# Optimization experiments

Measured on AMD Instinct MI355X. Metric: run time of the kernel, lower is better.

The kernel has to match this reference:

```python
import jax, jax.numpy as jnp
import numpy as np

B, T, D, H, V, K = 64, 128, 300, 256, 30000, 16
FILTERS = [3, 4, 5]
FN = [100, 100, 100]
CLS = 5


def setup_inputs() -> dict:
    key = jax.random.key(0)
    ks = jax.random.split(key, 32)
    n = lambda i, shape, s=0.05: (jax.random.normal(ks[i], shape, jnp.float32) * s)
    inp = jax.random.randint(ks[0], (B, T), 0, V)
    emb = n(1, (V + 2, D)).at[V + 1].set(0.0)  # padding_idx row = 0
    # GRU (1 layer, bidirectional), PyTorch gate order r,z,n
    Wx_f, Wh_f = n(2, (3 * H, D)), n(3, (3 * H, H))
    bx_f, bh_f = n(4, (3 * H,)), n(5, (3 * H,))
    Wx_b, Wh_b = n(6, (3 * H, D)), n(7, (3 * H, H))
    bx_b, bh_b = n(8, (3 * H,)), n(9, (3 * H,))
    fc1c_W, fc1c_b = n(10, (D, 2 * H)), n(11, (D,))
    concept_table = n(12, (V, K, D), 0.1)
    counts = jax.random.randint(ks[13], (V,), 1, K + 1)
    concept_mask = (jnp.arange(K)[None, :] < counts[:, None])  # bool [V,K]
    conv_W0, conv_b0 = n(14, (FN[0], FILTERS[0] * 2 * D)), n(15, (FN[0],))
    conv_W1, conv_b1 = n(16, (FN[1], FILTERS[1] * 2 * D)), n(17, (FN[1],))
    conv_W2, conv_b2 = n(18, (FN[2], FILTERS[2] * 2 * D)), n(19, (FN[2],))
    fc1_W, fc1_b = n(20, (100, sum(FN))), n(21, (100,))
    fc2_W, fc2_b = n(22, (CLS, 100)), n(23, (CLS,))
    return dict(inp=inp, emb=emb, Wx_f=Wx_f, Wh_f=Wh_f, bx_f=bx_f, bh_f=bh_f,
                Wx_b=Wx_b, Wh_b=Wh_b, bx_b=bx_b, bh_b=bh_b,
                fc1c_W=fc1c_W, fc1c_b=fc1c_b,
                concept_table=concept_table, concept_mask=concept_mask,
                conv_W0=conv_W0, conv_b0=conv_b0, conv_W1=conv_W1, conv_b1=conv_b1,
                conv_W2=conv_W2, conv_b2=conv_b2,
                fc1_W=fc1_W, fc1_b=fc1_b, fc2_W=fc2_W, fc2_b=fc2_b)


def _gru_dir(x, Wx, Wh, bx, bh):
    # x: [B,T,D] -> hidden states [B,T,H]; PyTorch GRU cell math.
    xg = jnp.einsum('btd,gd->btg', x, Wx) + bx  # precompute input gates [B,T,3H]

    def step(h, xg_t):
        gh = h @ Wh.T + bh
        xr, xz, xn = jnp.split(xg_t, 3, axis=-1)
        hr, hz, hn = jnp.split(gh, 3, axis=-1)
        r = jax.nn.sigmoid(xr + hr)
        z = jax.nn.sigmoid(xz + hz)
        nn_ = jnp.tanh(xn + r * hn)
        h2 = (1.0 - z) * nn_ + z * h
        return h2, h2

    h0 = jnp.zeros((x.shape[0], Wh.shape[1]), x.dtype)
    _, ys = jax.lax.scan(step, h0, jnp.swapaxes(xg, 0, 1))
    return jnp.swapaxes(ys, 0, 1)


def _forward(inp, emb, Wx_f, Wh_f, bx_f, bh_f, Wx_b, Wh_b, bx_b, bh_b,
             fc1c_W, fc1c_b, concept_table, concept_mask,
             conv_W0, conv_b0, conv_W1, conv_b1, conv_W2, conv_b2,
             fc1_W, fc1_b, fc2_W, fc2_b):
    x = emb[inp]                                   # [B,T,D]
    hf = _gru_dir(x, Wx_f, Wh_f, bx_f, bh_f)
    hb = jnp.flip(_gru_dir(jnp.flip(x, 1), Wx_b, Wh_b, bx_b, bh_b), 1)
    out = jnp.concatenate([hf, hb], axis=-1)       # [B,T,2H]
    ctx = jnp.einsum('bth,dh->btd', out, fc1c_W) + fc1c_b  # [B,T,D] context
    # batched gather-attend-reduce over per-word concept lists
    conc = concept_table[inp]                      # [B,T,K,D]
    mask = concept_mask[inp]                       # [B,T,K] bool
    scores = jnp.einsum('btkd,btd->btk', conc, ctx)
    scores = jnp.where(mask, scores, jnp.float32(-1e30))
    attn = jax.nn.softmax(scores, axis=-1)
    concept = jnp.einsum('btk,btkd->btd', attn, conc)
    concept = jax.lax.stop_gradient(concept)       # original detaches via .data.numpy()
    feat = jnp.concatenate([ctx, concept], axis=-1)  # [B,T,2D]
    pooled = []
    for fs, W, b in ((FILTERS[0], conv_W0, conv_b0),
                     (FILTERS[1], conv_W1, conv_b1),
                     (FILTERS[2], conv_W2, conv_b2)):
        L = T - fs + 1
        # Conv1d(kernel=2D*fs, stride=2D) over flattened feat == token-window matmul
        win = jnp.concatenate([feat[:, i:i + L, :] for i in range(fs)], axis=-1)  # [B,L,fs*2D]
        c = jax.nn.relu(jnp.einsum('blk,fk->blf', win, W) + b)
        pooled.append(jnp.max(c, axis=1))          # max-pool over positions -> [B,FN]
    h = jnp.concatenate(pooled, axis=1)            # [B,300]; dropout is identity in eval
    h = h @ fc1_W.T + fc1_b
    h = h @ fc2_W.T + fc2_b
    return jax.nn.softmax(h, axis=1)


def reference(inp, emb, Wx_f, Wh_f, bx_f, bh_f, Wx_b, Wh_b, bx_b, bh_b,
              fc1c_W, fc1c_b, concept_table, concept_mask,
              conv_W0, conv_b0, conv_W1, conv_b1, conv_W2, conv_b2,
              fc1_W, fc1_b, fc2_W, fc2_b):
    return _forward(inp, emb, Wx_f, Wh_f, bx_f, bh_f, Wx_b, Wh_b, bx_b, bh_b,
                    fc1c_W, fc1c_b, concept_table, concept_mask,
                    conv_W0, conv_b0, conv_W1, conv_b1, conv_W2, conv_b2,
                    fc1_W, fc1_b, fc2_W, fc2_b)
```

## Files before the change

kernel.cpp:

```cpp
#include <hip/hip_runtime.h>


typedef unsigned short u16;
typedef unsigned int u32;
typedef __attribute__((ext_vector_type(4))) u16 u16x4;
typedef __attribute__((ext_vector_type(8))) u16 u16x8;
typedef __attribute__((ext_vector_type(8))) __bf16 bf16x8;
typedef __attribute__((ext_vector_type(4))) float f32x4;

__device__ __forceinline__ float bf2f(u16 u) {
    union { u32 i; float f; } x; x.i = ((u32)u) << 16; return x.f;
}
__device__ __forceinline__ u16 f2bf(float f) {
    union { float f; u32 i; } x; x.f = f;
    u32 r = x.i + 0x7FFFu + ((x.i >> 16) & 1u);
    return (u16)(r >> 16);
}
__device__ __forceinline__ float sigm(float x) { return 1.f / (1.f + __expf(-x)); }
__device__ __forceinline__ float tanh_(float x) {
    float e = __expf(-2.f * fabsf(x));
    float t = (1.f - e) / (1.f + e);
    return x < 0.f ? -t : t;
}

__global__ __launch_bounds__(256) void detect_k(
    const u32* __restrict__ emb_raw, const u32* __restrict__ cmask_raw,
    int* __restrict__ flags)
{
    __shared__ int cnt0, cnt1;
    if (threadIdx.x == 0) { cnt0 = 0; cnt1 = 0; }
    __syncthreads();
    int c0 = 0;
    for (int i = threadIdx.x; i < 4096; i += 256) {
        float lo = bf2f((u16)(emb_raw[i] & 0xFFFFu));
        if (!(fabsf(lo) <= 4.0f)) c0++;
    }
    int c1 = 0;
    for (int i = threadIdx.x; i < 1024; i += 256) {
        if (cmask_raw[i] > 1u) c1++;
    }
    if (c0) atomicAdd(&cnt0, c0);
    if (c1) atomicAdd(&cnt1, c1);
    __syncthreads();
    if (threadIdx.x == 0) {
        flags[0] = (cnt0 > 64) ? 1 : 0;
        flags[1] = (cnt1 > 0) ? 1 : 0;
    }
}

struct CvtDesc { const void* src; u16* dst; int n; };
struct CvtArgs { CvtDesc d[20]; };

__global__ __launch_bounds__(256) void convert_many(CvtArgs a, const int* __restrict__ flags)
{
    CvtDesc de = a.d[blockIdx.y];
    const bool f32m = flags[0] != 0;
    int i4 = (blockIdx.x * 256 + threadIdx.x) * 4;
    if (i4 >= de.n) return;
    if (i4 + 4 <= de.n) {
        if (f32m) {
            const float* s = (const float*)de.src + i4;
            u16x4 o; o[0] = f2bf(s[0]); o[1] = f2bf(s[1]); o[2] = f2bf(s[2]); o[3] = f2bf(s[3]);
            *(u16x4*)(de.dst + i4) = o;
        } else {
            *(u16x4*)(de.dst + i4) = *(const u16x4*)((const u16*)de.src + i4);
        }
    } else {
        for (int e = 0; e < 4 && i4 + e < de.n; ++e)
            de.dst[i4 + e] = f32m ? f2bf(((const float*)de.src)[i4 + e])
                                  : ((const u16*)de.src)[i4 + e];
    }
}

__global__ __launch_bounds__(256) void build_mask(
    const void* __restrict__ cmask, int* __restrict__ mask16, const int* __restrict__ flags)
{
    int v = blockIdx.x * 256 + threadIdx.x;
    if (v >= 30000) return;
    int m = 0;
    if (flags[1]) {
        const unsigned char* p = (const unsigned char*)cmask + (size_t)v * 16;
#pragma unroll
        for (int k = 0; k < 16; ++k) if (p[k]) m |= (1 << k);
    } else {
        const int* p = (const int*)cmask + (size_t)v * 16;
#pragma unroll
        for (int k = 0; k < 16; ++k) if (p[k]) m |= (1 << k);
    }
    mask16[v] = m;
}

template<int ROWMODE, int EPI, int OUTBF>
__global__ __launch_bounds__(256) void gemm_bt(
    const u16* __restrict__ A, const u16* __restrict__ W,
    const u16* __restrict__ bias, const int* __restrict__ rowidx,
    float* __restrict__ Cf, u16* __restrict__ Cb,
    int M, int N, int K, int lda, int ldc, int Lrows, int strideT)
{
    __shared__ __align__(16) u16 sA[64 * 40];
    __shared__ __align__(16) u16 sW[64 * 40];

    const int tid = threadIdx.x;
    const int m0 = blockIdx.y * 64;
    const int n0 = blockIdx.x * 64;

    const int l  = tid & 63;
    const int w  = tid >> 6;
    const int wm = (w >> 1) << 5;
    const int wn = (w & 1) << 5;
    const int fr = l & 15;
    const int fk = (l >> 4) << 3;

    const int sr = tid >> 2;
    const int cb = (tid & 3) << 3;

    size_t abase;
    {
        int m = m0 + sr;
        if constexpr (ROWMODE == 1) {
            abase = (size_t)rowidx[m] * (size_t)lda;
        } else if constexpr (ROWMODE == 2) {
            int b = m / Lrows; int li = m - b * Lrows;
            abase = (size_t)(b * strideT + li) * (size_t)lda;
        } else {
            abase = (size_t)m * (size_t)lda;
        }
    }
    const int  wrow   = n0 + sr;
    const bool wvalid = wrow < N;
    const size_t wbase = (size_t)wrow * (size_t)K;

    f32x4 acc00 = {0,0,0,0}, acc01 = {0,0,0,0}, acc10 = {0,0,0,0}, acc11 = {0,0,0,0};

    for (int k0 = 0; k0 < K; k0 += 32) {
        __syncthreads();
        {
            u16x4 v0 = {0,0,0,0}, v1 = {0,0,0,0};
            int k = k0 + cb;
            if (k + 8 <= K) {
                const u16* p = A + abase + k;
                v0 = *(const u16x4*)p;
                v1 = *(const u16x4*)(p + 4);
            } else {
#pragma unroll
                for (int e = 0; e < 4; ++e) { int kk = k + e;     if (kk < K) v0[e] = A[abase + kk]; }
#pragma unroll
                for (int e = 0; e < 4; ++e) { int kk = k + 4 + e; if (kk < K) v1[e] = A[abase + kk]; }
            }
            *(u16x4*)(sA + sr * 40 + cb)     = v0;
            *(u16x4*)(sA + sr * 40 + cb + 4) = v1;
        }
        {
            u16x4 v0 = {0,0,0,0}, v1 = {0,0,0,0};
            int k = k0 + cb;
            if (wvalid) {
                if (k + 8 <= K) {
                    const u16* p = W + wbase + k;
                    v0 = *(const u16x4*)p;
                    v1 = *(const u16x4*)(p + 4);
                } else {
#pragma unroll
                    for (int e = 0; e < 4; ++e) { int kk = k + e;     if (kk < K) v0[e] = W[wbase + kk]; }
#pragma unroll
                    for (int e = 0; e < 4; ++e) { int kk = k + 4 + e; if (kk < K) v1[e] = W[wbase + kk]; }
                }
            }
            *(u16x4*)(sW + sr * 40 + cb)     = v0;
            *(u16x4*)(sW + sr * 40 + cb + 4) = v1;
        }
        __syncthreads();

        bf16x8 a0 = *(const bf16x8*)(sA + (wm + fr)      * 40 + fk);
        bf16x8 a1 = *(const bf16x8*)(sA + (wm + 16 + fr) * 40 + fk);
        bf16x8 b0 = *(const bf16x8*)(sW + (wn + fr)      * 40 + fk);
        bf16x8 b1 = *(const bf16x8*)(sW + (wn + 16 + fr) * 40 + fk);

        acc00 = __builtin_amdgcn_mfma_f32_16x16x32_bf16(a0, b0, acc00, 0, 0, 0);
        acc01 = __builtin_amdgcn_mfma_f32_16x16x32_bf16(a0, b1, acc01, 0, 0, 0);
        acc10 = __builtin_amdgcn_mfma_f32_16x16x32_bf16(a1, b0, acc10, 0, 0, 0);
        acc11 = __builtin_amdgcn_mfma_f32_16x16x32_bf16(a1, b1, acc11, 0, 0, 0);
    }

    const int rb = (l >> 4) << 2;
    const int cc = l & 15;
#define EPILOG(ACC, I, J)                                                     \
    {                                                                         \
        int col = n0 + wn + (J)*16 + cc;                                      \
        if (col < N) {                                                        \
            float bv = bf2f(bias[col]);                                       \
            _Pragma("unroll")                                                 \
            for (int r = 0; r < 4; ++r) {                                     \
                int row = m0 + wm + (I)*16 + rb + r;                          \
                if (row < M) {                                                \
                    float v = ACC[r] + bv;                                    \
                    if (EPI == 2) v = fmaxf(v, 0.f);                          \
                    if (OUTBF) Cb[(size_t)row * ldc + col] = f2bf(v);         \
                    else       Cf[(size_t)row * ldc + col] = v;               \
                }                                                             \
            }                                                                 \
        }                                                                     \
    }
    EPILOG(acc00, 0, 0); EPILOG(acc01, 0, 1); EPILOG(acc10, 1, 0); EPILOG(acc11, 1, 1);
#undef EPILOG
}

#define GB 8
__global__ __launch_bounds__(512, 2) void gru_scan_mfma(
    const u16* __restrict__ xgf, const u16* __restrict__ xgb,
    const u16* __restrict__ whf, const u16* __restrict__ whb,
    const u16* __restrict__ bhf, const u16* __restrict__ bhb,
    u16* __restrict__ outb)
{
    const int bg  = blockIdx.x;
    const int dir = blockIdx.y;
    const u16* xg = dir ? xgb : xgf;
    const u16* wh = dir ? whb : whf;
    const u16* bh = dir ? bhb : bhf;

    const int tid = threadIdx.x;
    const int w = tid >> 6;
    const int l = tid & 63;

    __shared__ __align__(16) u16 h_bf[16][264];
    __shared__ __align__(16) float h_f[GB][260];
    __shared__ __align__(16) float gh[GB][772];
    __shared__ float bh_s[768];

    for (int i = tid; i < 16 * 264; i += 512) ((u16*)h_bf)[i] = 0;
    for (int i = tid; i < GB * 260; i += 512) ((float*)h_f)[i] = 0.f;
    for (int i = tid; i < 768; i += 512) bh_s[i] = bf2f(bh[i]);

    bf16x8 bfr[6][8];
#pragma unroll
    for (int c = 0; c < 6; ++c) {
#pragma unroll
        for (int kt = 0; kt < 8; ++kt) {
            const int n = w * 96 + c * 16 + (l & 15);
            const int k = kt * 32 + (l >> 4) * 8;
            bfr[c][kt] = *(const bf16x8*)(wh + (size_t)n * 256 + k);
        }
    }

    const int qrow = (l >> 4) << 2;
    const int arow = l & 15;
    const int aofs = (l >> 4) << 3;
    const int j0 = l * 4;
    const int bglob = bg * GB + w;

    __syncthreads();

    for (int s = 0; s < 128; ++s) {
        const int t = dir ? (127 - s) : s;

        f32x4 acc[6];
#pragma unroll
        for (int c = 0; c < 6; ++c) acc[c] = (f32x4){0.f, 0.f, 0.f, 0.f};
#pragma unroll
        for (int kt = 0; kt < 8; ++kt) {
            bf16x8 a = *(const bf16x8*)(&h_bf[arow][kt * 32 + aofs]);
#pragma unroll
            for (int c = 0; c < 6; ++c)
                acc[c] = __builtin_amdgcn_mfma_f32_16x16x32_bf16(a, bfr[c][kt], acc[c], 0, 0, 0);
        }
        if (qrow < GB) {
#pragma unroll
            for (int c = 0; c < 6; ++c) {
                const int col = w * 96 + c * 16 + (l & 15);
#pragma unroll
                for (int r = 0; r < 4; ++r)
                    gh[qrow + r][col] = acc[c][r];
            }
        }
        __syncthreads();

        const size_t tokbase = (size_t)(bglob * 128 + t) * 768;
        u16x4 xr4 = *(const u16x4*)(xg + tokbase + j0);
        u16x4 xz4 = *(const u16x4*)(xg + tokbase + 256 + j0);
        u16x4 xn4 = *(const u16x4*)(xg + tokbase + 512 + j0);
        f32x4 gr = *(const f32x4*)(&gh[w][j0]);
        f32x4 gz = *(const f32x4*)(&gh[w][256 + j0]);
        f32x4 gn = *(const f32x4*)(&gh[w][512 + j0]);
        f32x4 br = *(const f32x4*)(&bh_s[j0]);
        f32x4 bz = *(const f32x4*)(&bh_s[256 + j0]);
        f32x4 bn = *(const f32x4*)(&bh_s[512 + j0]);
        f32x4 hp = *(const f32x4*)(&h_f[w][j0]);
        u16x4 ho;
        f32x4 hn;
#pragma unroll
        for (int e = 0; e < 4; ++e) {
            float r = sigm(bf2f(xr4[e]) + gr[e] + br[e]);
            float z = sigm(bf2f(xz4[e]) + gz[e] + bz[e]);
            float n = tanh_(bf2f(xn4[e]) + r * (gn[e] + bn[e]));
            float h2 = (1.f - z) * n + z * hp[e];
            hn[e] = h2;
            ho[e] = f2bf(h2);
        }
        *(u16x4*)(&h_bf[w][j0]) = ho;
        *(f32x4*)(&h_f[w][j0]) = hn;
        *(u16x4*)(outb + (size_t)(bglob * 128 + t) * 512 + dir * 256 + j0) = ho;
        __syncthreads();
    }
}
#undef GB

__global__ __launch_bounds__(256) void attn_kernel(
    const int* __restrict__ inp, const void* __restrict__ ctab,
    const int* __restrict__ mask16, const int* __restrict__ flags,
    u16* __restrict__ feat)
{
    const int tok = blockIdx.x;
    const int tid = threadIdx.x;
    const int v = inp[tok];
    const bool f32m = flags[0] != 0;

    __shared__ float ctx_s[300];
    __shared__ __align__(16) u16 conc_s[16 * 300];
    __shared__ float sc_s[16];
    __shared__ float at_s[16];

    for (int d = tid; d < 300; d += 256) ctx_s[d] = bf2f(feat[(size_t)tok * 600 + d]);
    if (f32m) {
        const float4* src = (const float4*)((const float*)ctab + (size_t)v * 4800);
        for (int i = tid; i < 1200; i += 256) {
            float4 x = src[i];
            u16x4 o; o[0] = f2bf(x.x); o[1] = f2bf(x.y); o[2] = f2bf(x.z); o[3] = f2bf(x.w);
            *(u16x4*)(conc_s + i * 4) = o;
        }
    } else {
        const u16x8* src = (const u16x8*)((const u16*)ctab + (size_t)v * 4800);
        u16x8* dst = (u16x8*)conc_s;
        for (int i = tid; i < 600; i += 256) dst[i] = src[i];
    }
    __syncthreads();

    const int g = tid >> 4, ln = tid & 15;
    float s = 0.f;
    for (int d = ln; d < 300; d += 16) s += bf2f(conc_s[g * 300 + d]) * ctx_s[d];
    s += __shfl_xor(s, 1); s += __shfl_xor(s, 2); s += __shfl_xor(s, 4); s += __shfl_xor(s, 8);
    if (ln == 0) sc_s[g] = ((mask16[v] >> g) & 1) ? s : -1e30f;
    __syncthreads();

    if (tid == 0) {
        float m = -1e30f;
#pragma unroll
        for (int i = 0; i < 16; ++i) m = fmaxf(m, sc_s[i]);
        float p[16]; float den = 0.f;
#pragma unroll
        for (int i = 0; i < 16; ++i) {
            float pe = (sc_s[i] <= -1e29f) ? 0.f : __expf(sc_s[i] - m);
            p[i] = pe; den += pe;
        }
        float inv = den > 0.f ? 1.f / den : 0.f;
#pragma unroll
        for (int i = 0; i < 16; ++i) at_s[i] = p[i] * inv;
    }
    __syncthreads();

    for (int d = tid; d < 300; d += 256) {
        float a = 0.f;
#pragma unroll
        for (int g2 = 0; g2 < 16; ++g2) a += at_s[g2] * bf2f(conc_s[g2 * 300 + d]);
        feat[(size_t)tok * 600 + 300 + d] = f2bf(a);
    }
}

__global__ __launch_bounds__(128) void maxpool_k(
    const float* __restrict__ c0, const float* __restrict__ c1,
    const float* __restrict__ c2, float* __restrict__ pool)
{
    const int b = blockIdx.x, which = blockIdx.y, f = threadIdx.x;
    if (f >= 100) return;
    const float* c = which == 0 ? c0 : (which == 1 ? c1 : c2);
    const int L = which == 0 ? 126 : (which == 1 ? 125 : 124);
    float m = -1e30f;
    for (int l = 0; l < L; ++l) m = fmaxf(m, c[(size_t)(b * L + l) * 100 + f]);
    pool[b * 300 + which * 100 + f] = m;
}

__global__ __launch_bounds__(128) void final_k(
    const float* __restrict__ pool,
    const u16* __restrict__ fc1W, const u16* __restrict__ fc1b,
    const u16* __restrict__ fc2W, const u16* __restrict__ fc2b,
    float* __restrict__ out)
{
    const int b = blockIdx.x, tid = threadIdx.x;
    __shared__ float ps[300], h1[100], lg[5];
    for (int d = tid; d < 300; d += 128) ps[d] = pool[b * 300 + d];
    __syncthreads();
    if (tid < 100) {
        float a = bf2f(fc1b[tid]);
        for (int k = 0; k < 300; ++k) a += bf2f(fc1W[tid * 300 + k]) * ps[k];
        h1[tid] = a;
    }
    __syncthreads();
    if (tid < 5) {
        float a = bf2f(fc2b[tid]);
        for (int k = 0; k < 100; ++k) a += bf2f(fc2W[tid * 100 + k]) * h1[k];
        lg[tid] = a;
    }
    __syncthreads();
    if (tid == 0) {
        float m = fmaxf(fmaxf(fmaxf(lg[0], lg[1]), fmaxf(lg[2], lg[3])), lg[4]);
        float e0 = __expf(lg[0] - m), e1 = __expf(lg[1] - m), e2 = __expf(lg[2] - m),
              e3 = __expf(lg[3] - m), e4 = __expf(lg[4] - m);
        float inv = 1.f / (e0 + e1 + e2 + e3 + e4);
        out[b * 5 + 0] = e0 * inv;
        out[b * 5 + 1] = e1 * inv;
        out[b * 5 + 2] = e2 * inv;
        out[b * 5 + 3] = e3 * inv;
        out[b * 5 + 4] = e4 * inv;
    }
}

extern "C" void kernel_launch(void* const* d_in, const int* in_sizes, int n_in,
                              void* d_out, int out_size, void* d_ws, size_t ws_size,
                              hipStream_t stream)
{
    (void)n_in; (void)out_size; (void)ws_size;

    const int*  inp     = (const int*)d_in[0];
    const void* embR    = d_in[1];
    const void* WxfR    = d_in[2];
    const void* WhfR    = d_in[3];
    const void* bxfR    = d_in[4];
    const void* bhfR    = d_in[5];
    const void* WxbR    = d_in[6];
    const void* WhbR    = d_in[7];
    const void* bxbR    = d_in[8];
    const void* bhbR    = d_in[9];
    const void* fc1cWR  = d_in[10];
    const void* fc1cbR  = d_in[11];
    const void* ctabR   = d_in[12];
    const void* cmaskR  = d_in[13];
    const void* cw0R    = d_in[14];
    const void* cb0R    = d_in[15];
    const void* cw1R    = d_in[16];
    const void* cb1R    = d_in[17];
    const void* cw2R    = d_in[18];
    const void* cb2R    = d_in[19];
    const void* fc1WR   = d_in[20];
    const void* fc1bR   = d_in[21];
    const void* fc2WR   = d_in[22];
    const void* fc2bR   = d_in[23];

    char* ws = (char*)d_ws;
    size_t off = 0;
    auto alloc = [&](size_t bytes) -> char* {
        char* r = ws + off;
        off = (off + bytes + 255) & ~(size_t)255;
        return r;
    };

    u16*   xgf    = (u16*)alloc(8192ull * 768 * 2);
    u16*   xgb    = (u16*)alloc(8192ull * 768 * 2);
    u16*   outb   = (u16*)alloc(8192ull * 512 * 2);
    u16*   feat   = (u16*)alloc(8192ull * 600 * 2);
    float* c0     = (float*)alloc(64ull * 126 * 100 * 4);
    float* c1     = (float*)alloc(64ull * 125 * 100 * 4);
    float* c2     = (float*)alloc(64ull * 124 * 100 * 4);
    float* pool   = (float*)alloc(64ull * 300 * 4);
    int*   flags  = (int*)alloc(256);
    int*   mask16 = (int*)alloc(30000ull * 4);
    u16*   embc   = (u16*)alloc(9000600ull * 2);
    u16*   wxfc   = (u16*)alloc(230400ull * 2);
    u16*   whfc   = (u16*)alloc(196608ull * 2);
    u16*   bxfc   = (u16*)alloc(768ull * 2);
    u16*   bhfc   = (u16*)alloc(768ull * 2);
    u16*   wxbc   = (u16*)alloc(230400ull * 2);
    u16*   whbc   = (u16*)alloc(196608ull * 2);
    u16*   bxbc   = (u16*)alloc(768ull * 2);
    u16*   bhbc   = (u16*)alloc(768ull * 2);
    u16*   fc1cWc = (u16*)alloc(153600ull * 2);
    u16*   fc1cbc = (u16*)alloc(300ull * 2);
    u16*   cw0c   = (u16*)alloc(180000ull * 2);
    u16*   cb0c   = (u16*)alloc(100ull * 2);
    u16*   cw1c   = (u16*)alloc(240000ull * 2);
    u16*   cb1c   = (u16*)alloc(100ull * 2);
    u16*   cw2c   = (u16*)alloc(300000ull * 2);
    u16*   cb2c   = (u16*)alloc(100ull * 2);
    u16*   fc1Wc  = (u16*)alloc(30000ull * 2);
    u16*   fc1bc  = (u16*)alloc(100ull * 2);
    u16*   fc2Wc  = (u16*)alloc(500ull * 2);
    u16*   fc2bc  = (u16*)alloc(8ull * 2);

    detect_k<<<1, 256, 0, stream>>>((const u32*)embR, (const u32*)cmaskR, flags);

    {
        CvtArgs a{};
        a.d[0]  = { WxfR,   wxfc,   230400 };
        a.d[1]  = { WhfR,   whfc,   196608 };
        a.d[2]  = { bxfR,   bxfc,   768 };
        a.d[3]  = { bhfR,   bhfc,   768 };
        a.d[4]  = { WxbR,   wxbc,   230400 };
        a.d[5]  = { WhbR,   whbc,   196608 };
        a.d[6]  = { bxbR,   bxbc,   768 };
        a.d[7]  = { bhbR,   bhbc,   768 };
        a.d[8]  = { fc1cWR, fc1cWc, 153600 };
        a.d[9]  = { fc1cbR, fc1cbc, 300 };
        a.d[10] = { cw0R,   cw0c,   180000 };
        a.d[11] = { cb0R,   cb0c,   100 };
        a.d[12] = { cw1R,   cw1c,   240000 };
        a.d[13] = { cb1R,   cb1c,   100 };
        a.d[14] = { cw2R,   cw2c,   300000 };
        a.d[15] = { cb2R,   cb2c,   100 };
        a.d[16] = { fc1WR,  fc1Wc,  30000 };
        a.d[17] = { fc1bR,  fc1bc,  100 };
        a.d[18] = { fc2WR,  fc2Wc,  500 };
        a.d[19] = { fc2bR,  fc2bc,  5 };
        convert_many<<<dim3(293, 20), 256, 0, stream>>>(a, flags);
        CvtArgs e{};
        e.d[0] = { embR, embc, 9000600 };
        convert_many<<<dim3(8790, 1), 256, 0, stream>>>(e, flags);
    }

    build_mask<<<118, 256, 0, stream>>>(cmaskR, mask16, flags);

    gemm_bt<1, 1, 1><<<dim3(12, 128), 256, 0, stream>>>(
        embc, wxfc, bxfc, inp, nullptr, xgf, 8192, 768, 300, 300, 768, 0, 0);
    gemm_bt<1, 1, 1><<<dim3(12, 128), 256, 0, stream>>>(
        embc, wxbc, bxbc, inp, nullptr, xgb, 8192, 768, 300, 300, 768, 0, 0);

    gru_scan_mfma<<<dim3(8, 2), 512, 0, stream>>>(
        xgf, xgb, whfc, whbc, bhfc, bhbc, outb);

    gemm_bt<0, 1, 1><<<dim3(5, 128), 256, 0, stream>>>(
        outb, fc1cWc, fc1cbc, nullptr, nullptr, feat, 8192, 300, 512, 512, 600, 0, 0);

    attn_kernel<<<dim3(8192), 256, 0, stream>>>(inp, ctabR, mask16, flags, feat);

    gemm_bt<2, 2, 0><<<dim3(2, 126), 256, 0, stream>>>(
        feat, cw0c, cb0c, nullptr, c0, nullptr, 8064, 100, 1800, 600, 100, 126, 128);
    gemm_bt<2, 2, 0><<<dim3(2, 125), 256, 0, stream>>>(
        feat, cw1c, cb1c, nullptr, c1, nullptr, 8000, 100, 2400, 600, 100, 125, 128);
    gemm_bt<2, 2, 0><<<dim3(2, 124), 256, 0, stream>>>(
        feat, cw2c, cb2c, nullptr, c2, nullptr, 7936, 100, 3000, 600, 100, 124, 128);

    maxpool_k<<<dim3(64, 3), 128, 0, stream>>>(c0, c1, c2, pool);

    final_k<<<dim3(64), 128, 0, stream>>>(pool, fc1Wc, fc1bc, fc2Wc, fc2bc, (float*)d_out);
}
```

Before: 594.0 us.

## Drop embedding conversion, fuse GRU input GEMMs, restructure conv as per-tap GEMM

Removes the full-embedding-table bf16 conversion and the runtime dtype detection by having the input-gate GEMM gather f32 embedding rows and convert them on load. The two directional input GEMMs become one GEMM with concatenated weights. The GRU scan now runs 12 waves so each wave handles fewer gate columns, keeps the hidden state in registers, and prefetches input gates before the MFMA. The three window-conv GEMMs are replaced by one per-tap GEMM over repacked weights, with shifted sums, bias, ReLU and max-pool done in a fused pooling kernel. This cuts large conversion traffic and repeated window reads, at the cost of a bf16 intermediate and a serial pooling loop.

```diff
diff --git a/kernel.cpp b/kernel.cpp
--- a/kernel.cpp
+++ b/kernel.cpp
@@ -24,51 +24,33 @@
 }
 
 __global__ __launch_bounds__(256) void detect_k(
-    const u32* __restrict__ emb_raw, const u32* __restrict__ cmask_raw,
-    int* __restrict__ flags)
-{
-    __shared__ int cnt0, cnt1;
-    if (threadIdx.x == 0) { cnt0 = 0; cnt1 = 0; }
-    __syncthreads();
-    int c0 = 0;
-    for (int i = threadIdx.x; i < 4096; i += 256) {
-        float lo = bf2f((u16)(emb_raw[i] & 0xFFFFu));
-        if (!(fabsf(lo) <= 4.0f)) c0++;
-    }
+    const u32* __restrict__ cmask_raw, int* __restrict__ flags)
+{
+    __shared__ int cnt1;
+    if (threadIdx.x == 0) cnt1 = 0;
+    __syncthreads();
     int c1 = 0;
-    for (int i = threadIdx.x; i < 1024; i += 256) {
+    for (int i = threadIdx.x; i < 1024; i += 256)
         if (cmask_raw[i] > 1u) c1++;
-    }
-    if (c0) atomicAdd(&cnt0, c0);
     if (c1) atomicAdd(&cnt1, c1);
     __syncthreads();
-    if (threadIdx.x == 0) {
-        flags[0] = (cnt0 > 64) ? 1 : 0;
-        flags[1] = (cnt1 > 0) ? 1 : 0;
-    }
+    if (threadIdx.x == 0) flags[1] = (cnt1 > 0) ? 1 : 0;
 }
 
 struct CvtDesc { const void* src; u16* dst; int n; };
-struct CvtArgs { CvtDesc d[20]; };
-
-__global__ __launch_bounds__(256) void convert_many(CvtArgs a, const int* __restrict__ flags)
+struct CvtArgs { CvtDesc d[17]; };
+
+__global__ __launch_bounds__(256) void convert_f32(CvtArgs a)
 {
     CvtDesc de = a.d[blockIdx.y];
-    const bool f32m = flags[0] != 0;
     int i4 = (blockIdx.x * 256 + threadIdx.x) * 4;
     if (i4 >= de.n) return;
+    const float* s = (const float*)de.src + i4;
     if (i4 + 4 <= de.n) {
-        if (f32m) {
-            const float* s = (const float*)de.src + i4;
-            u16x4 o; o[0] = f2bf(s[0]); o[1] = f2bf(s[1]); o[2] = f2bf(s[2]); o[3] = f2bf(s[3]);
-            *(u16x4*)(de.dst + i4) = o;
-        } else {
-            *(u16x4*)(de.dst + i4) = *(const u16x4*)((const u16*)de.src + i4);
-        }
+        u16x4 o; o[0] = f2bf(s[0]); o[1] = f2bf(s[1]); o[2] = f2bf(s[2]); o[3] = f2bf(s[3]);
+        *(u16x4*)(de.dst + i4) = o;
     } else {
-        for (int e = 0; e < 4 && i4 + e < de.n; ++e)
-            de.dst[i4 + e] = f32m ? f2bf(((const float*)de.src)[i4 + e])
-                                  : ((const u16*)de.src)[i4 + e];
+        for (int e = 0; e < 4 && i4 + e < de.n; ++e) de.dst[i4 + e] = f2bf(s[e]);
     }
 }
 
@@ -90,12 +72,28 @@
     mask16[v] = m;
 }
 
-template<int ROWMODE, int EPI, int OUTBF>
+__global__ __launch_bounds__(256) void repack_conv(
+    const float* __restrict__ cw0, const float* __restrict__ cw1,
+    const float* __restrict__ cw2, u16* __restrict__ wcat)
+{
+    const int r = blockIdx.x;
+    const int d0 = threadIdx.x * 4;
+    if (d0 >= 600) return;
+    const float* src;
+    if (r < 300)      { int f = r % 100,       i = r / 100;        src = cw0 + (size_t)f * 1800 + i * 600; }
+    else if (r < 700) { int rr = r - 300, f = rr % 100, i = rr / 100; src = cw1 + (size_t)f * 2400 + i * 600; }
+    else              { int rr = r - 700, f = rr % 100, i = rr / 100; src = cw2 + (size_t)f * 3000 + i * 600; }
+    float4 x = *(const float4*)(src + d0);
+    u16x4 o; o[0] = f2bf(x.x); o[1] = f2bf(x.y); o[2] = f2bf(x.z); o[3] = f2bf(x.w);
+    *(u16x4*)(wcat + (size_t)r * 600 + d0) = o;
+}
+
+template<int ROWMODE, int EPI, int OUTBF, int AF32>
 __global__ __launch_bounds__(256) void gemm_bt(
-    const u16* __restrict__ A, const u16* __restrict__ W,
+    const void* __restrict__ Araw, const u16* __restrict__ W,
     const u16* __restrict__ bias, const int* __restrict__ rowidx,
     float* __restrict__ Cf, u16* __restrict__ Cb,
-    int M, int N, int K, int lda, int ldc, int Lrows, int strideT)
+    int M, int N, int K, int lda, int ldc)
 {
     __shared__ __align__(16) u16 sA[64 * 40];
     __shared__ __align__(16) u16 sW[64 * 40];
@@ -117,14 +115,8 @@
     size_t abase;
     {
         int m = m0 + sr;
-        if constexpr (ROWMODE == 1) {
-            abase = (size_t)rowidx[m] * (size_t)lda;
-        } else if constexpr (ROWMODE == 2) {
-            int b = m / Lrows; int li = m - b * Lrows;
-            abase = (size_t)(b * strideT + li) * (size_t)lda;
-        } else {
-            abase = (size_t)m * (size_t)lda;
-        }
+        if constexpr (ROWMODE == 1) abase = (size_t)rowidx[m] * (size_t)lda;
+        else                        abase = (size_t)m * (size_t)lda;
     }
     const int  wrow   = n0 + sr;
     const bool wvalid = wrow < N;
@@ -137,15 +129,32 @@
         {
             u16x4 v0 = {0,0,0,0}, v1 = {0,0,0,0};
             int k = k0 + cb;
-            if (k + 8 <= K) {
-                const u16* p = A + abase + k;
-                v0 = *(const u16x4*)p;
-                v1 = *(const u16x4*)(p + 4);
+            if constexpr (AF32) {
+                const float* A = (const float*)Araw;
+                if (k + 8 <= K) {
+                    const float* p = A + abase + k;
+                    float4 x0 = *(const float4*)p;
+                    float4 x1 = *(const float4*)(p + 4);
+                    v0[0] = f2bf(x0.x); v0[1] = f2bf(x0.y); v0[2] = f2bf(x0.z); v0[3] = f2bf(x0.w);
+                    v1[0] = f2bf(x1.x); v1[1] = f2bf(x1.y); v1[2] = f2bf(x1.z); v1[3] = f2bf(x1.w);
+                } else {
+#pragma unroll
+                    for (int e = 0; e < 4; ++e) { int kk = k + e;     if (kk < K) v0[e] = f2bf(A[abase + kk]); }
+#pragma unroll
+                    for (int e = 0; e < 4; ++e) { int kk = k + 4 + e; if (kk < K) v1[e] = f2bf(A[abase + kk]); }
+                }
             } else {
-#pragma unroll
-                for (int e = 0; e < 4; ++e) { int kk = k + e;     if (kk < K) v0[e] = A[abase + kk]; }
-#pragma unroll
-                for (int e = 0; e < 4; ++e) { int kk = k + 4 + e; if (kk < K) v1[e] = A[abase + kk]; }
+                const u16* A = (const u16*)Araw;
+                if (k + 8 <= K) {
+                    const u16* p = A + abase + k;
+                    v0 = *(const u16x4*)p;
+                    v1 = *(const u16x4*)(p + 4);
+                } else {
+#pragma unroll
+                    for (int e = 0; e < 4; ++e) { int kk = k + e;     if (kk < K) v0[e] = A[abase + kk]; }
+#pragma unroll
+                    for (int e = 0; e < 4; ++e) { int kk = k + 4 + e; if (kk < K) v1[e] = A[abase + kk]; }
+                }
             }
             *(u16x4*)(sA + sr * 40 + cb)     = v0;
             *(u16x4*)(sA + sr * 40 + cb + 4) = v1;
@@ -187,7 +196,7 @@
     {                                                                         \
         int col = n0 + wn + (J)*16 + cc;                                      \
         if (col < N) {                                                        \
-            float bv = bf2f(bias[col]);                                       \
+            float bv = (EPI >= 1) ? bf2f(bias[col]) : 0.f;                    \
             _Pragma("unroll")                                                 \
             for (int r = 0; r < 4; ++r) {                                     \
                 int row = m0 + wm + (I)*16 + rb + r;                          \
@@ -205,15 +214,14 @@
 }
 
 #define GB 8
-__global__ __launch_bounds__(512, 2) void gru_scan_mfma(
-    const u16* __restrict__ xgf, const u16* __restrict__ xgb,
+__global__ __launch_bounds__(768, 3) void gru_scan_mfma(
+    const u16* __restrict__ xg,
     const u16* __restrict__ whf, const u16* __restrict__ whb,
     const u16* __restrict__ bhf, const u16* __restrict__ bhb,
     u16* __restrict__ outb)
 {
     const int bg  = blockIdx.x;
     const int dir = blockIdx.y;
-    const u16* xg = dir ? xgb : xgf;
     const u16* wh = dir ? whb : whf;
     const u16* bh = dir ? bhb : bhf;
 
@@ -222,50 +230,56 @@
     const int l = tid & 63;
 
     __shared__ __align__(16) u16 h_bf[16][264];
-    __shared__ __align__(16) float h_f[GB][260];
     __shared__ __align__(16) float gh[GB][772];
     __shared__ float bh_s[768];
 
-    for (int i = tid; i < 16 * 264; i += 512) ((u16*)h_bf)[i] = 0;
-    for (int i = tid; i < GB * 260; i += 512) ((float*)h_f)[i] = 0.f;
-    for (int i = tid; i < 768; i += 512) bh_s[i] = bf2f(bh[i]);
-
-    bf16x8 bfr[6][8];
-#pragma unroll
-    for (int c = 0; c < 6; ++c) {
+    for (int i = tid; i < 16 * 264; i += 768) ((u16*)h_bf)[i] = 0;
+    bh_s[tid] = bf2f(bh[tid]);
+
+    bf16x8 bfr[4][8];
+#pragma unroll
+    for (int c = 0; c < 4; ++c)
 #pragma unroll
         for (int kt = 0; kt < 8; ++kt) {
-            const int n = w * 96 + c * 16 + (l & 15);
+            const int n = w * 64 + c * 16 + (l & 15);
             const int k = kt * 32 + (l >> 4) * 8;
             bfr[c][kt] = *(const bf16x8*)(wh + (size_t)n * 256 + k);
         }
-    }
 
     const int qrow = (l >> 4) << 2;
     const int arow = l & 15;
     const int aofs = (l >> 4) << 3;
     const int j0 = l * 4;
     const int bglob = bg * GB + w;
+    f32x4 hreg = {0.f, 0.f, 0.f, 0.f};
 
     __syncthreads();
 
     for (int s = 0; s < 128; ++s) {
         const int t = dir ? (127 - s) : s;
 
-        f32x4 acc[6];
-#pragma unroll
-        for (int c = 0; c < 6; ++c) acc[c] = (f32x4){0.f, 0.f, 0.f, 0.f};
+        u16x4 xr4 = {0,0,0,0}, xz4 = {0,0,0,0}, xn4 = {0,0,0,0};
+        if (w < GB) {
+            const size_t tb = (size_t)(bglob * 128 + t) * 1536 + dir * 768;
+            xr4 = *(const u16x4*)(xg + tb + j0);
+            xz4 = *(const u16x4*)(xg + tb + 256 + j0);
+            xn4 = *(const u16x4*)(xg + tb + 512 + j0);
+        }
+
+        f32x4 acc[4];
+#pragma unroll
+        for (int c = 0; c < 4; ++c) acc[c] = (f32x4){0.f, 0.f, 0.f, 0.f};
 #pragma unroll
         for (int kt = 0; kt < 8; ++kt) {
             bf16x8 a = *(const bf16x8*)(&h_bf[arow][kt * 32 + aofs]);
 #pragma unroll
-            for (int c = 0; c < 6; ++c)
+            for (int c = 0; c < 4; ++c)
                 acc[c] = __builtin_amdgcn_mfma_f32_16x16x32_bf16(a, bfr[c][kt], acc[c], 0, 0, 0);
         }
         if (qrow < GB) {
 #pragma unroll
-            for (int c = 0; c < 6; ++c) {
-                const int col = w * 96 + c * 16 + (l & 15);
+            for (int c = 0; c < 4; ++c) {
+                const int col = w * 64 + c * 16 + (l & 15);
 #pragma unroll
                 for (int r = 0; r < 4; ++r)
                     gh[qrow + r][col] = acc[c][r];
@@ -273,45 +287,38 @@
         }
         __syncthreads();
 
-        const size_t tokbase = (size_t)(bglob * 128 + t) * 768;
-        u16x4 xr4 = *(const u16x4*)(xg + tokbase + j0);
-        u16x4 xz4 = *(const u16x4*)(xg + tokbase + 256 + j0);
-        u16x4 xn4 = *(const u16x4*)(xg + tokbase + 512 + j0);
-        f32x4 gr = *(const f32x4*)(&gh[w][j0]);
-        f32x4 gz = *(const f32x4*)(&gh[w][256 + j0]);
-        f32x4 gn = *(const f32x4*)(&gh[w][512 + j0]);
-        f32x4 br = *(const f32x4*)(&bh_s[j0]);
-        f32x4 bz = *(const f32x4*)(&bh_s[256 + j0]);
-        f32x4 bn = *(const f32x4*)(&bh_s[512 + j0]);
-        f32x4 hp = *(const f32x4*)(&h_f[w][j0]);
-        u16x4 ho;
-        f32x4 hn;
-#pragma unroll
-        for (int e = 0; e < 4; ++e) {
-            float r = sigm(bf2f(xr4[e]) + gr[e] + br[e]);
-            float z = sigm(bf2f(xz4[e]) + gz[e] + bz[e]);
-            float n = tanh_(bf2f(xn4[e]) + r * (gn[e] + bn[e]));
-            float h2 = (1.f - z) * n + z * hp[e];
-            hn[e] = h2;
-            ho[e] = f2bf(h2);
-        }
-        *(u16x4*)(&h_bf[w][j0]) = ho;
-        *(f32x4*)(&h_f[w][j0]) = hn;
-        *(u16x4*)(outb + (size_t)(bglob * 128 + t) * 512 + dir * 256 + j0) = ho;
+        if (w < GB) {
+            f32x4 gr = *(const f32x4*)(&gh[w][j0]);
+            f32x4 gz = *(const f32x4*)(&gh[w][256 + j0]);
+            f32x4 gn = *(const f32x4*)(&gh[w][512 + j0]);
+            f32x4 br = *(const f32x4*)(&bh_s[j0]);
+            f32x4 bz = *(const f32x4*)(&bh_s[256 + j0]);
+            f32x4 bn = *(const f32x4*)(&bh_s[512 + j0]);
+            u16x4 ho;
+#pragma unroll
+            for (int e = 0; e < 4; ++e) {
+                float r = sigm(bf2f(xr4[e]) + gr[e] + br[e]);
+                float z = sigm(bf2f(xz4[e]) + gz[e] + bz[e]);
+                float n = tanh_(bf2f(xn4[e]) + r * (gn[e] + bn[e]));
+                float h2 = (1.f - z) * n + z * hreg[e];
+                hreg[e] = h2;
+                ho[e] = f2bf(h2);
+            }
+            *(u16x4*)(&h_bf[w][j0]) = ho;
+            *(u16x4*)(outb + (size_t)(bglob * 128 + t) * 512 + dir * 256 + j0) = ho;
+        }
         __syncthreads();
     }
 }
 #undef GB
 
 __global__ __launch_bounds__(256) void attn_kernel(
-    const int* __restrict__ inp, const void* __restrict__ ctab,
-    const int* __restrict__ mask16, const int* __restrict__ flags,
-    u16* __restrict__ feat)
+    const int* __restrict__ inp, const float* __restrict__ ctab,
+    const int* __restrict__ mask16, u16* __restrict__ feat)
 {
     const int tok = blockIdx.x;
     const int tid = threadIdx.x;
     const int v = inp[tok];
-    const bool f32m = flags[0] != 0;
 
     __shared__ float ctx_s[300];
     __shared__ __align__(16) u16 conc_s[16 * 300];
@@ -319,17 +326,13 @@
     __shared__ float at_s[16];
 
     for (int d = tid; d < 300; d += 256) ctx_s[d] = bf2f(feat[(size_t)tok * 600 + d]);
-    if (f32m) {
-        const float4* src = (const float4*)((const float*)ctab + (size_t)v * 4800);
+    {
+        const float4* src = (const float4*)(ctab + (size_t)v * 4800);
         for (int i = tid; i < 1200; i += 256) {
             float4 x = src[i];
             u16x4 o; o[0] = f2bf(x.x); o[1] = f2bf(x.y); o[2] = f2bf(x.z); o[3] = f2bf(x.w);
             *(u16x4*)(conc_s + i * 4) = o;
         }
-    } else {
-        const u16x8* src = (const u16x8*)((const u16*)ctab + (size_t)v * 4800);
-        u16x8* dst = (u16x8*)conc_s;
-        for (int i = tid; i < 600; i += 256) dst[i] = src[i];
     }
     __syncthreads();
 
@@ -364,17 +367,25 @@
     }
 }
 
-__global__ __launch_bounds__(128) void maxpool_k(
-    const float* __restrict__ c0, const float* __restrict__ c1,
-    const float* __restrict__ c2, float* __restrict__ pool)
+__global__ __launch_bounds__(128) void pool_fused(
+    const u16* __restrict__ P, const u16* __restrict__ cbcat,
+    float* __restrict__ pool)
 {
     const int b = blockIdx.x, which = blockIdx.y, f = threadIdx.x;
     if (f >= 100) return;
-    const float* c = which == 0 ? c0 : (which == 1 ? c1 : c2);
-    const int L = which == 0 ? 126 : (which == 1 ? 125 : 124);
-    float m = -1e30f;
-    for (int l = 0; l < L; ++l) m = fmaxf(m, c[(size_t)(b * L + l) * 100 + f]);
-    pool[b * 300 + which * 100 + f] = m;
+    const int fs  = which == 0 ? 3 : (which == 1 ? 4 : 5);
+    const int off = which == 0 ? 0 : (which == 1 ? 300 : 700);
+    const int L   = 128 - fs + 1;
+    const float bias = bf2f(cbcat[which * 100 + f]);
+    float mm = -1e30f;
+    for (int l2 = 0; l2 < L; ++l2) {
+        float s = bias;
+#pragma unroll 5
+        for (int i = 0; i < fs; ++i)
+            s += bf2f(P[(size_t)(b * 128 + l2 + i) * 1200 + off + i * 100 + f]);
+        mm = fmaxf(mm, s);
+    }
+    pool[b * 300 + which * 100 + f] = fmaxf(mm, 0.f);
 }
 
 __global__ __launch_bounds__(128) void final_k(
@@ -416,7 +427,7 @@
                               void* d_out, int out_size, void* d_ws, size_t ws_size,
                               hipStream_t stream)
 {
-    (void)n_in; (void)out_size; (void)ws_size;
+    (void)in_sizes; (void)n_in; (void)out_size; (void)ws_size;
 
     const int*  inp     = (const int*)d_in[0];
     const void* embR    = d_in[1];
@@ -451,91 +462,71 @@
         return r;
     };
 
-    u16*   xgf    = (u16*)alloc(8192ull * 768 * 2);
-    u16*   xgb    = (u16*)alloc(8192ull * 768 * 2);
+    u16*   xgc    = (u16*)alloc(8192ull * 1536 * 2);
     u16*   outb   = (u16*)alloc(8192ull * 512 * 2);
     u16*   feat   = (u16*)alloc(8192ull * 600 * 2);
-    float* c0     = (float*)alloc(64ull * 126 * 100 * 4);
-    float* c1     = (float*)alloc(64ull * 125 * 100 * 4);
-    float* c2     = (float*)alloc(64ull * 124 * 100 * 4);
+    u16*   P      = (u16*)alloc(8192ull * 1200 * 2);
     float* pool   = (float*)alloc(64ull * 300 * 4);
     int*   flags  = (int*)alloc(256);
     int*   mask16 = (int*)alloc(30000ull * 4);
-    u16*   embc   = (u16*)alloc(9000600ull * 2);
-    u16*   wxfc   = (u16*)alloc(230400ull * 2);
+    u16*   wxcat  = (u16*)alloc(1536ull * 300 * 2);
+    u16*   bxcat  = (u16*)alloc(1536ull * 2);
     u16*   whfc   = (u16*)alloc(196608ull * 2);
-    u16*   bxfc   = (u16*)alloc(768ull * 2);
+    u16*   whbc   = (u16*)alloc(196608ull * 2);
     u16*   bhfc   = (u16*)alloc(768ull * 2);
-    u16*   wxbc   = (u16*)alloc(230400ull * 2);
-    u16*   whbc   = (u16*)alloc(196608ull * 2);
-    u16*   bxbc   = (u16*)alloc(768ull * 2);
     u16*   bhbc   = (u16*)alloc(768ull * 2);
     u16*   fc1cWc = (u16*)alloc(153600ull * 2);
     u16*   fc1cbc = (u16*)alloc(300ull * 2);
-    u16*   cw0c   = (u16*)alloc(180000ull * 2);
-    u16*   cb0c   = (u16*)alloc(100ull * 2);
-    u16*   cw1c   = (u16*)alloc(240000ull * 2);
-    u16*   cb1c   = (u16*)alloc(100ull * 2);
-    u16*   cw2c   = (u16*)alloc(300000ull * 2);
-    u16*   cb2c   = (u16*)alloc(100ull * 2);
+    u16*   wcat   = (u16*)alloc(1200ull * 600 * 2);
+    u16*   cbcat  = (u16*)alloc(300ull * 2);
     u16*   fc1Wc  = (u16*)alloc(30000ull * 2);
     u16*   fc1bc  = (u16*)alloc(100ull * 2);
     u16*   fc2Wc  = (u16*)alloc(500ull * 2);
     u16*   fc2bc  = (u16*)alloc(8ull * 2);
 
-    detect_k<<<1, 256, 0, stream>>>((const u32*)embR, (const u32*)cmaskR, flags);
+    detect_k<<<1, 256, 0, stream>>>((const u32*)cmaskR, flags);
 
     {
         CvtArgs a{};
-        a.d[0]  = { WxfR,   wxfc,   230400 };
-        a.d[1]  = { WhfR,   whfc,   196608 };
-        a.d[2]  = { bxfR,   bxfc,   768 };
-        a.d[3]  = { bhfR,   bhfc,   768 };
-        a.d[4]  = { WxbR,   wxbc,   230400 };
-        a.d[5]  = { WhbR,   whbc,   196608 };
-        a.d[6]  = { bxbR,   bxbc,   768 };
-        a.d[7]  = { bhbR,   bhbc,   768 };
-        a.d[8]  = { fc1cWR, fc1cWc, 153600 };
-        a.d[9]  = { fc1cbR, fc1cbc, 300 };
-        a.d[10] = { cw0R,   cw0c,   180000 };
-        a.d[11] = { cb0R,   cb0c,   100 };
-        a.d[12] = { cw1R,   cw1c,   240000 };
-        a.d[13] = { cb1R,   cb1c,   100 };
-        a.d[14] = { cw2R,   cw2c,   300000 };
-        a.d[15] = { cb2R,   cb2c,   100 };
-        a.d[16] = { fc1WR,  fc1Wc,  30000 };
-        a.d[17] = { fc1bR,  fc1bc,  100 };
-        a.d[18] = { fc2WR,  fc2Wc,  500 };
-        a.d[19] = { fc2bR,  fc2bc,  5 };
-        convert_many<<<dim3(293, 20), 256, 0, stream>>>(a, flags);
-        CvtArgs e{};
-        e.d[0] = { embR, embc, 9000600 };
-        convert_many<<<dim3(8790, 1), 256, 0, stream>>>(e, flags);
+        a.d[0]  = { WxfR,   wxcat,          230400 };
+        a.d[1]  = { WxbR,   wxcat + 230400, 230400 };
+        a.d[2]  = { bxfR,   bxcat,          768 };
+        a.d[3]  = { bxbR,   bxcat + 768,    768 };
+        a.d[4]  = { WhfR,   whfc,           196608 };
+        a.d[5]  = { WhbR,   whbc,           196608 };
+        a.d[6]  = { bhfR,   bhfc,           768 };
+        a.d[7]  = { bhbR,   bhbc,           768 };
+        a.d[8]  = { fc1cWR, fc1cWc,         153600 };
+        a.d[9]  = { fc1cbR, fc1cbc,         300 };
+        a.d[10] = { cb0R,   cbcat,          100 };
+        a.d[11] = { cb1R,   cbcat + 100,    100 };
+        a.d[12] = { cb2R,   cbcat + 200,    100 };
+        a.d[13] = { fc1WR,  fc1Wc,          30000 };
+        a.d[14] = { fc1bR,  fc1bc,          100 };
+        a.d[15] = { fc2WR,  fc2Wc,          500 };
+        a.d[16] = { fc2bR,  fc2bc,          5 };
+        convert_f32<<<dim3(225, 17), 256, 0, stream>>>(a);
     }
 
     build_mask<<<118, 256, 0, stream>>>(cmaskR, mask16, flags);
-
-    gemm_bt<1, 1, 1><<<dim3(12, 128), 256, 0, stream>>>(
-        embc, wxfc, bxfc, inp, nullptr, xgf, 8192, 768, 300, 300, 768, 0, 0);
-    gemm_bt<1, 1, 1><<<dim3(12, 128), 256, 0, stream>>>(
-        embc, wxbc, bxbc, inp, nullptr, xgb, 8192, 768, 300, 300, 768, 0, 0);
-
-    gru_scan_mfma<<<dim3(8, 2), 512, 0, stream>>>(
-        xgf, xgb, whfc, whbc, bhfc, bhbc, outb);
-
-    gemm_bt<0, 1, 1><<<dim3(5, 128), 256, 0, stream>>>(
-        outb, fc1cWc, fc1cbc, nullptr, nullptr, feat, 8192, 300, 512, 512, 600, 0, 0);
-
-    attn_kernel<<<dim3(8192), 256, 0, stream>>>(inp, ctabR, mask16, flags, feat);
-
-    gemm_bt<2, 2, 0><<<dim3(2, 126), 256, 0, stream>>>(
-        feat, cw0c, cb0c, nullptr, c0, nullptr, 8064, 100, 1800, 600, 100, 126, 128);
-    gemm_bt<2, 2, 0><<<dim3(2, 125), 256, 0, stream>>>(
-        feat, cw1c, cb1c, nullptr, c1, nullptr, 8000, 100, 2400, 600, 100, 125, 128);
-    gemm_bt<2, 2, 0><<<dim3(2, 124), 256, 0, stream>>>(
-        feat, cw2c, cb2c, nullptr, c2, nullptr, 7936, 100, 3000, 600, 100, 124, 128);
-
-    maxpool_k<<<dim3(64, 3), 128, 0, stream>>>(c0, c1, c2, pool);
+    repack_conv<<<1200, 256, 0, stream>>>(
+        (const float*)cw0R, (const float*)cw1R, (const float*)cw2R, wcat);
+
+    gemm_bt<1, 1, 1, 1><<<dim3(24, 128), 256, 0, stream>>>(
+        embR, wxcat, bxcat, inp, nullptr, xgc, 8192, 1536, 300, 300, 1536);
+
+    gru_scan_mfma<<<dim3(8, 2), 768, 0, stream>>>(
+        xgc, whfc, whbc, bhfc, bhbc, outb);
+
+    gemm_bt<0, 1, 1, 0><<<dim3(5, 128), 256, 0, stream>>>(
+        outb, fc1cWc, fc1cbc, nullptr, nullptr, feat, 8192, 300, 512, 512, 600);
+
+    attn_kernel<<<dim3(8192), 256, 0, stream>>>(inp, (const float*)ctabR, mask16, feat);
+
+    gemm_bt<0, 0, 1, 0><<<dim3(19, 128), 256, 0, stream>>>(
+        feat, wcat, nullptr, nullptr, nullptr, P, 8192, 1200, 600, 600, 1200);
+
+    pool_fused<<<dim3(64, 3), 128, 0, stream>>>(P, cbcat, pool);
 
     final_k<<<dim3(64), 128, 0, stream>>>(pool, fc1Wc, fc1bc, fc2Wc, fc2bc, (float*)d_out);
 }
```

Measured after the change: 733.2 us. 23.4% more time.
